# Kernel optimization log

Hardware: AMD Instinct MI355X
Metric: run time of the kernel (lower is better)

Reference implementation:

```python
import jax, jax.numpy as jnp
import numpy as np

T, B, D = 2048, 16, 1024
DELTA_INIT = -2.0

def _xavier(key, shape, gain=1.0):
    fan_in, fan_out = shape[1], shape[0]
    limit = gain * np.sqrt(6.0 / (fan_in + fan_out))
    return jax.random.uniform(key, shape, jnp.float32, -limit, limit)

def setup_inputs() -> dict:
    key = jax.random.key(0)
    ks = jax.random.split(key, 4)
    return {
        "x": jax.random.normal(ks[0], (T, B, D), jnp.float32),
        "h0": jnp.zeros((B, D), jnp.float32),
        "W_x": _xavier(ks[1], (D, D)),
        "r_h": jnp.zeros((D,), jnp.float32),
        "W_delta": _xavier(ks[2], (D, D), gain=0.1),
        "W_gate": _xavier(ks[3], (D, D)),
        "b": jnp.zeros((D,), jnp.float32),
        "b_delta": jnp.full((D,), DELTA_INIT, jnp.float32),
        "b_gate": jnp.zeros((D,), jnp.float32),
    }

def reference(x, h0, W_x, r_h, W_delta, W_gate, b, b_delta, b_gate):
    # Precompute input projections as batched GEMMs (independent of h):
    delta = jax.nn.sigmoid(jnp.einsum('tbd,ed->tbe', x, W_delta) + b_delta)  # [T,B,D]
    cand_x = jnp.einsum('tbd,ed->tbe', x, W_x) + b                            # [T,B,D]
    gate = jax.nn.silu(jnp.einsum('tbd,ed->tbe', x, W_gate) + b_gate)        # [T,B,D]

    def step(h_prev, inp):
        d_t, cx_t = inp
        cand = jnp.tanh(cx_t + r_h * h_prev)
        h_new = (1.0 - d_t) * h_prev + d_t * cand
        return h_new, h_new

    _, h_seq = jax.lax.scan(step, h0, (delta, cand_x))  # h_seq: [T,B,D]
    output = h_seq * gate
    h = jnp.concatenate([h0[None], h_seq], axis=0)  # [T+1,B,D]
    return output, h
```

## Files before the change

### kernel.cpp

```cpp
#include <hip/hip_runtime.h>
#include <hip/hip_bf16.h>

#define T_DIM 2048
#define B_DIM 16
#define D_DIM 1024
#define M_DIM (T_DIM * B_DIM)
#define K_DIM D_DIM
#define N_DIM (3 * D_DIM)
#define BD (B_DIM * D_DIM)
#define CHUNKS 64
#define CLEN (T_DIM / CHUNKS)
#define NT (K_DIM / 64)

typedef __attribute__((ext_vector_type(8))) short bf16x8;
typedef __attribute__((ext_vector_type(4))) float f32x4;
typedef __attribute__((ext_vector_type(4))) unsigned short us4;
typedef __attribute__((ext_vector_type(8))) unsigned short us8;

__device__ __forceinline__ unsigned short f2bf(float f) {
    unsigned int u = __builtin_bit_cast(unsigned int, f);
    u += 0x7fffu + ((u >> 16) & 1u);
    return (unsigned short)(u >> 16);
}
__device__ __forceinline__ float bf2f(unsigned short s) {
    unsigned int u = ((unsigned int)s) << 16;
    return __builtin_bit_cast(float, u);
}
__device__ __forceinline__ float sigmoid_f(float x) {
    return __builtin_amdgcn_rcpf(1.0f + __expf(-x));
}
__device__ __forceinline__ float tanh_f(float x) {
    float e = __expf(2.0f * x);
    return 1.0f - 2.0f * __builtin_amdgcn_rcpf(e + 1.0f);
}

__device__ __forceinline__ void gload_lds16(const unsigned short* g, unsigned short* l) {
    __builtin_amdgcn_global_load_lds(
        (const __attribute__((address_space(1))) unsigned int*)g,
        (__attribute__((address_space(3))) unsigned int*)l, 16, 0, 0);
}

__device__ __forceinline__ bf16x8 lds_rd(const unsigned short* lds, int slot, int srow, int kk, int lk) {
    int ce = (((kk * 64) + (lk * 16)) ^ ((srow & 7) << 4)) >> 1;
    return *reinterpret_cast<const bf16x8*>(lds + slot * 8192 + srow * 64 + ce);
}

#define XN8 (M_DIM * K_DIM / 8)
#define WN8 (D_DIM * K_DIM / 8)
__global__ __launch_bounds__(256)
void conv_all(const float* __restrict__ x,  const float* __restrict__ Wx,
              const float* __restrict__ Wd, const float* __restrict__ Wg,
              unsigned short* __restrict__ xb, unsigned short* __restrict__ Wb)
{
    int i = blockIdx.x * 256 + threadIdx.x;
    const float* src;
    unsigned short* dst;
    int off;
    if (i < XN8)                { src = x;  dst = xb;               off = i; }
    else if (i < XN8 + WN8)     { src = Wx; dst = Wb;               off = i - XN8; }
    else if (i < XN8 + 2 * WN8) { src = Wd; dst = Wb + (size_t)WN8 * 8;     off = i - XN8 - WN8; }
    else                        { src = Wg; dst = Wb + (size_t)2 * WN8 * 8; off = i - XN8 - 2 * WN8; }
    const f32x4* p = reinterpret_cast<const f32x4*>(src) + (size_t)off * 2;
    f32x4 v0 = __builtin_nontemporal_load(p);
    f32x4 v1 = __builtin_nontemporal_load(p + 1);
    us8 w;
    w[0] = f2bf(v0[0]); w[1] = f2bf(v0[1]); w[2] = f2bf(v0[2]); w[3] = f2bf(v0[3]);
    w[4] = f2bf(v1[0]); w[5] = f2bf(v1[1]); w[6] = f2bf(v1[2]); w[7] = f2bf(v1[3]);
    *reinterpret_cast<us8*>(dst + (size_t)off * 8) = w;
}

__global__ __launch_bounds__(512, 2)
void gemm_fused(const unsigned short* __restrict__ xb,
                const unsigned short* __restrict__ Wb,
                const float* __restrict__ bx, const float* __restrict__ bdl,
                const float* __restrict__ bg,
                unsigned short* __restrict__ cxw, unsigned short* __restrict__ dw,
                unsigned short* __restrict__ gw)
{
    __shared__ unsigned short lds[8 * 8192];
    unsigned short* ldsA = lds;
    unsigned short* ldsB = lds + 4 * 8192;

    const int NWG = (M_DIM / 256) * (N_DIM / 256);
    int bid = blockIdx.x;
    int wg  = (bid & 7) * (NWG / 8) + (bid >> 3);
    const int bidM = wg / 12;
    const int bidN = wg % 12;
    const int tM  = bidM * 256;
    const int tN  = bidN * 256;
    const int arr = tN >> 10;
    const int nb  = tN & 1023;

    const float* bias = (arr == 0) ? bx : (arr == 1) ? bdl : bg;
    unsigned short* outp = (arr == 0) ? cxw : (arr == 1) ? dw : gw;

    const int tid  = threadIdx.x;
    const int lane = tid & 63;
    const int wid  = tid >> 6;
    const int wr = wid >> 2, wc = wid & 3;
    const int lr = lane & 15, lk = lane >> 4;

    const unsigned short* Asrc = xb + (size_t)tM * K_DIM;
    const unsigned short* Bsrc = Wb + (size_t)arr * (D_DIM * K_DIM) + (size_t)nb * K_DIM;

    const int t8 = tid >> 3;
    const int ke = (((tid & 7) ^ (t8 & 7)) << 3);
    auto arow = [&](int h, int w) {
        int s = w * 64 + t8;
        return ((s >> 4) & 1) * 128 + (h * 4 + (s >> 5)) * 16 + (s & 15);
    };
    const int rA00 = arow(0, 0), rA01 = arow(0, 1);
    const int rA10 = arow(1, 0), rA11 = arow(1, 1);

    auto stA = [&](int t, int r0, int r1, int slot) {
        gload_lds16(Asrc + (size_t)r0 * K_DIM + t * 64 + ke, ldsA + slot * 8192 + wid * 512);
        gload_lds16(Asrc + (size_t)r1 * K_DIM + t * 64 + ke, ldsA + slot * 8192 + 4096 + wid * 512);
    };
    auto stB = [&](int t, int h, int slot) {
        gload_lds16(Bsrc + (size_t)(h * 128 + t8) * K_DIM + t * 64 + ke,      ldsB + slot * 8192 + wid * 512);
        gload_lds16(Bsrc + (size_t)(h * 128 + 64 + t8) * K_DIM + t * 64 + ke, ldsB + slot * 8192 + 4096 + wid * 512);
    };

    f32x4 acc[8][4];
#pragma unroll
    for (int mi = 0; mi < 8; mi++)
#pragma unroll
        for (int ni = 0; ni < 4; ni++)
            acc[mi][ni] = (f32x4){0.f, 0.f, 0.f, 0.f};

    stA(0, rA00, rA01, 0);
    stA(0, rA10, rA11, 1);
    stB(0, 0, 0);
    stB(0, 1, 1);
    stB(1, 0, 2);
    stA(1, rA00, rA01, 2);
    stB(1, 1, 3);
    asm volatile("s_waitcnt vmcnt(6)" ::: "memory");
    __builtin_amdgcn_s_barrier();

    const int brow = (wc & 1) * 64;
    bf16x8 bf[4][2], afP[2][2], afQ[2][2];

#define RD_AF(DST, P, ASLOT)                                                       \
    do {                                                                           \
        _Pragma("unroll") for (int j = 0; j < 2; j++)                              \
            _Pragma("unroll") for (int kk = 0; kk < 2; kk++)                       \
                DST[j][kk] = lds_rd(ldsA, (ASLOT),                                 \
                                    ((2 * (P) + j) & 3) * 32 + wr * 16 + lr, kk, lk); \
    } while (0)

#define RD_BF(BSLOT)                                                               \
    do {                                                                           \
        _Pragma("unroll") for (int ni = 0; ni < 4; ni++)                           \
            _Pragma("unroll") for (int kk = 0; kk < 2; kk++)                       \
                bf[ni][kk] = lds_rd(ldsB, (BSLOT), brow + ni * 16 + lr, kk, lk);   \
    } while (0)

#define MFMA8(P, AF)                                                               \
    do {                                                                           \
        __builtin_amdgcn_s_setprio(1);                                             \
        _Pragma("unroll") for (int j = 0; j < 2; j++)                              \
            _Pragma("unroll") for (int ni = 0; ni < 4; ni++) {                     \
                acc[2 * (P) + j][ni] = __builtin_amdgcn_mfma_f32_16x16x32_bf16(    \
                    bf[ni][0], AF[j][0], acc[2 * (P) + j][ni], 0, 0, 0);           \
                acc[2 * (P) + j][ni] = __builtin_amdgcn_mfma_f32_16x16x32_bf16(    \
                    bf[ni][1], AF[j][1], acc[2 * (P) + j][ni], 0, 0, 0);           \
            }                                                                      \
        __builtin_amdgcn_s_setprio(0);                                             \
    } while (0)

#define SCHED0 __builtin_amdgcn_sched_barrier(0)
#define BAR    __builtin_amdgcn_s_barrier()

#define TILE(KT, PAR, LAST)                                                        \
    do {                                                                           \
        const int a0s = 2 * (PAR), a1s = 2 * (PAR) + 1;                            \
             \
        if ((KT) + 1 < NT) stA((KT) + 1, rA10, rA11, 2 * (1 - (PAR)) + 1);         \
        RD_AF(afQ, 1, a0s);                                                        \
        SCHED0;                                                                    \
        MFMA8(0, afP);                                                             \
        BAR;                                                                       \
                                                                          \
        if ((KT) + 2 < NT) stB((KT) + 2, 0, 2 * (PAR));                            \
        RD_AF(afP, 2, a1s);                                                        \
        SCHED0;                                                                    \
        MFMA8(1, afQ);                                                             \
        BAR;                                                                       \
                                                                          \
        if ((KT) + 2 < NT) stA((KT) + 2, rA00, rA01, 2 * (PAR));                   \
        RD_AF(afQ, 3, a1s);                                                        \
        SCHED0;                                                                    \
        MFMA8(2, afP);                                                             \
        BAR;                                                                       \
           \
           \
        if ((KT) + 2 < NT) stB((KT) + 2, 1, 2 * (PAR) + 1);                        \
        if ((KT) < NT - 2) asm volatile("s_waitcnt vmcnt(6)" ::: "memory");        \
        else               asm volatile("s_waitcnt vmcnt(0)" ::: "memory");        \
        BAR;                                                                       \
        MFMA8(3, afQ);                                                             \
        if (!(LAST)) {                                                             \
            RD_BF(2 * (1 - (PAR)) + (wc >> 1));                                    \
            RD_AF(afP, 0, 2 * (1 - (PAR)));                                        \
        }                                                                          \
        BAR;                                                                       \
    } while (0)

    RD_BF(wc >> 1);
    RD_AF(afP, 0, 0);

    for (int kt = 0; kt < NT; kt += 2) {
        TILE(kt, 0, false);
        TILE(kt + 1, 1, (kt + 1 == NT - 1));
    }

#pragma unroll
    for (int mi = 0; mi < 8; mi++) {
        int row = wr * 128 + mi * 16 + lr;
#pragma unroll
        for (int ni = 0; ni < 4; ni++) {
            int col0 = wc * 64 + ni * 16 + lk * 4;
            f32x4 bia = *reinterpret_cast<const f32x4*>(bias + nb + col0);
            us4 w;
#pragma unroll
            for (int r = 0; r < 4; r++) {
                float v = acc[mi][ni][r] + bia[r];
                if (arr == 1)      v = sigmoid_f(v);
                else if (arr == 2) v = v * sigmoid_f(v);
                w[r] = f2bf(v);
            }
            int byte = (row * 512 + col0 * 2) ^ ((row & 7) << 4);
            *reinterpret_cast<us4*>(reinterpret_cast<char*>(lds) + byte) = w;
        }
    }
    __syncthreads();
#pragma unroll
    for (int it = 0; it < 16; ++it) {
        int off8 = it * 512 + tid;
        int row  = off8 >> 5;
        int col8 = (off8 & 31) << 3;
        int byte = (row * 512 + col8 * 2) ^ ((row & 7) << 4);
        us8 v = *reinterpret_cast<const us8*>(reinterpret_cast<char*>(lds) + byte);
        __builtin_nontemporal_store(v,
            reinterpret_cast<us8*>(outp + (size_t)(tM + row) * D_DIM + nb + col8));
    }
#undef RD_AF
#undef RD_BF
#undef MFMA8
#undef SCHED0
#undef BAR
#undef TILE
}

__global__ __launch_bounds__(256)
void scan_pass1(const unsigned short* __restrict__ dw,
                const unsigned short* __restrict__ cxw,
                float* __restrict__ Aw, float* __restrict__ Bw)
{
    int g  = blockIdx.x * 256 + threadIdx.x;
    int c  = g / (BD / 4);
    int i0 = (g % (BD / 4)) * 4;
    size_t base = (size_t)c * CLEN * BD + i0;

    float a[4]  = {1.f, 1.f, 1.f, 1.f};
    float hb[4] = {0.f, 0.f, 0.f, 0.f};
    for (int t = 0; t < CLEN; t++) {
        us4 dv = *reinterpret_cast<const us4*>(dw  + base + (size_t)t * BD);
        us4 cv = *reinterpret_cast<const us4*>(cxw + base + (size_t)t * BD);
#pragma unroll
        for (int j = 0; j < 4; j++) {
            float d = bf2f(dv[j]);
            float om = 1.f - d;
            float cand = tanh_f(bf2f(cv[j]));
            hb[j] = om * hb[j] + d * cand;
            a[j] *= om;
        }
    }
    f32x4 av = {a[0], a[1], a[2], a[3]};
    f32x4 bv = {hb[0], hb[1], hb[2], hb[3]};
    *reinterpret_cast<f32x4*>(Aw + (size_t)c * BD + i0) = av;
    *reinterpret_cast<f32x4*>(Bw + (size_t)c * BD + i0) = bv;
}

__global__ __launch_bounds__(256)
void scan_pass2(const float* __restrict__ Aw, const float* __restrict__ Bw,
                const float* __restrict__ h0, float* __restrict__ hin,
                float* __restrict__ hseq)
{
    int i0 = (blockIdx.x * 256 + threadIdx.x) * 4;
    if (i0 >= BD) return;
    f32x4 h = *reinterpret_cast<const f32x4*>(h0 + i0);
    *reinterpret_cast<f32x4*>(hseq + i0) = h;
    for (int c = 0; c < CHUNKS; c++) {
        *reinterpret_cast<f32x4*>(hin + (size_t)c * BD + i0) = h;
        f32x4 A  = *reinterpret_cast<const f32x4*>(Aw + (size_t)c * BD + i0);
        f32x4 Bv = *reinterpret_cast<const f32x4*>(Bw + (size_t)c * BD + i0);
        h = A * h + Bv;
    }
}

__global__ __launch_bounds__(256)
void scan_pass3(const unsigned short* __restrict__ dw,
                const unsigned short* __restrict__ cxw,
                const unsigned short* __restrict__ gw,
                const float* __restrict__ hin,
                float* __restrict__ out, float* __restrict__ hseq)
{
    int g  = blockIdx.x * 256 + threadIdx.x;
    int c  = g / (BD / 4);
    int i0 = (g % (BD / 4)) * 4;
    size_t base = (size_t)c * CLEN * BD + i0;

    f32x4 h4 = *reinterpret_cast<const f32x4*>(hin + (size_t)c * BD + i0);
    float h[4] = {h4[0], h4[1], h4[2], h4[3]};
    for (int t = 0; t < CLEN; t++) {
        size_t idx = base + (size_t)t * BD;
        us4 dv = *reinterpret_cast<const us4*>(dw  + idx);
        us4 cv = *reinterpret_cast<const us4*>(cxw + idx);
        us4 gv = *reinterpret_cast<const us4*>(gw  + idx);
        f32x4 o, hv;
#pragma unroll
        for (int j = 0; j < 4; j++) {
            float d = bf2f(dv[j]);
            float om = 1.f - d;
            float cand = tanh_f(bf2f(cv[j]));
            h[j] = om * h[j] + d * cand;
            o[j] = h[j] * bf2f(gv[j]);
            hv[j] = h[j];
        }
        __builtin_nontemporal_store(o,  reinterpret_cast<f32x4*>(out + idx));
        __builtin_nontemporal_store(hv, reinterpret_cast<f32x4*>(hseq + idx + BD));
    }
}

__global__ __launch_bounds__(256)
void scan_fixup(const float* __restrict__ rh, const float* __restrict__ h0,
                const unsigned short* __restrict__ dw,
                const unsigned short* __restrict__ cxw,
                const unsigned short* __restrict__ gw,
                float* __restrict__ out, float* __restrict__ hseq)
{
    int i = blockIdx.x * 256 + threadIdx.x;
    if (i >= BD) return;
    float r = rh[i & (D_DIM - 1)];
    if (r == 0.0f) return;
    float h = h0[i];
    for (int t = 0; t < T_DIM; t++) {
        size_t idx = (size_t)t * BD + i;
        float d = bf2f(dw[idx]);
        float cand = tanh_f(bf2f(cxw[idx]) + r * h);
        h = (1.f - d) * h + d * cand;
        out[idx] = h * bf2f(gw[idx]);
        hseq[idx + BD] = h;
    }
}

extern "C" void kernel_launch(void* const* d_in, const int* in_sizes, int n_in,
                              void* d_out, int out_size, void* d_ws, size_t ws_size,
                              hipStream_t stream)
{
    const float* x   = (const float*)d_in[0];
    const float* h0  = (const float*)d_in[1];
    const float* Wx  = (const float*)d_in[2];
    const float* rh  = (const float*)d_in[3];
    const float* Wd  = (const float*)d_in[4];
    const float* Wg  = (const float*)d_in[5];
    const float* bx  = (const float*)d_in[6];
    const float* bdl = (const float*)d_in[7];
    const float* bg  = (const float*)d_in[8];

    float* out  = (float*)d_out;
    float* hseq = out + (size_t)T_DIM * BD;

    unsigned short* dw  = (unsigned short*)d_ws;
    unsigned short* cxw = dw  + (size_t)M_DIM * D_DIM;
    unsigned short* gw  = cxw + (size_t)M_DIM * D_DIM;
    float* Aw  = (float*)(gw + (size_t)M_DIM * D_DIM);
    float* Bw  = Aw + (size_t)CHUNKS * BD;
    float* hin = Bw + (size_t)CHUNKS * BD;

    unsigned short* xb = (unsigned short*)d_out;
    unsigned short* Wb = xb + (size_t)M_DIM * K_DIM;

    conv_all<<<dim3((XN8 + 3 * WN8) / 256), dim3(256), 0, stream>>>(x, Wx, Wd, Wg, xb, Wb);

    gemm_fused<<<dim3((M_DIM / 256) * (N_DIM / 256)), dim3(512), 0, stream>>>(
        xb, Wb, bx, bdl, bg, cxw, dw, gw);

    scan_pass1<<<dim3(CHUNKS * BD / 4 / 256), dim3(256), 0, stream>>>(dw, cxw, Aw, Bw);
    scan_pass2<<<dim3(BD / 4 / 256 + 1), dim3(256), 0, stream>>>(Aw, Bw, h0, hin, hseq);
    scan_pass3<<<dim3(CHUNKS * BD / 4 / 256), dim3(256), 0, stream>>>(dw, cxw, gw, hin, out, hseq);
    scan_fixup<<<dim3(BD / 256), dim3(256), 0, stream>>>(rh, h0, dw, cxw, gw, out, hseq);
}
```

Baseline: 373.4 us.

## Collapse GEMM k-tile pipeline into two phases with full A-fragment loads

Restructures the bf16 MFMA main loop of the projection GEMM. The old version used four phases per k-tile, ping-ponging A fragments between two register sets and separating phases with sched barriers. The new version has two phases: it loads all four A fragments for one half of the tile, then issues 32 MFMAs, and groups the next-tile A/B global-to-LDS loads into one block. This cuts barriers per tile and drops the scheduling fences, but gives up the explicit overlap of LDS reads with MFMA work and raises register pressure. The prologue now waits for all outstanding loads instead of leaving some in flight.

```diff
diff --git a/kernel.cpp b/kernel.cpp
--- a/kernel.cpp
+++ b/kernel.cpp
@@ -132,21 +132,20 @@
     stA(0, rA10, rA11, 1);
     stB(0, 0, 0);
     stB(0, 1, 1);
+    stA(1, rA00, rA01, 2);
     stB(1, 0, 2);
-    stA(1, rA00, rA01, 2);
     stB(1, 1, 3);
-    asm volatile("s_waitcnt vmcnt(6)" ::: "memory");
+    asm volatile("s_waitcnt vmcnt(0)" ::: "memory");
     __builtin_amdgcn_s_barrier();
 
     const int brow = (wc & 1) * 64;
-    bf16x8 bf[4][2], afP[2][2], afQ[2][2];
-
-#define RD_AF(DST, P, ASLOT)                                                       \
+    bf16x8 bf[4][2], af[4][2];
+
+#define RD_AF8(ASLOT)                                                              \
     do {                                                                           \
-        _Pragma("unroll") for (int j = 0; j < 2; j++)                              \
+        _Pragma("unroll") for (int m4 = 0; m4 < 4; m4++)                           \
             _Pragma("unroll") for (int kk = 0; kk < 2; kk++)                       \
-                DST[j][kk] = lds_rd(ldsA, (ASLOT),                                 \
-                                    ((2 * (P) + j) & 3) * 32 + wr * 16 + lr, kk, lk); \
+                af[m4][kk] = lds_rd(ldsA, (ASLOT), m4 * 32 + wr * 16 + lr, kk, lk); \
     } while (0)
 
 #define RD_BF(BSLOT)                                                               \
@@ -156,59 +155,44 @@
                 bf[ni][kk] = lds_rd(ldsB, (BSLOT), brow + ni * 16 + lr, kk, lk);   \
     } while (0)
 
-#define MFMA8(P, AF)                                                               \
+#define MFMA32(HALF)                                                               \
     do {                                                                           \
         __builtin_amdgcn_s_setprio(1);                                             \
-        _Pragma("unroll") for (int j = 0; j < 2; j++)                              \
+        _Pragma("unroll") for (int m4 = 0; m4 < 4; m4++)                           \
             _Pragma("unroll") for (int ni = 0; ni < 4; ni++) {                     \
-                acc[2 * (P) + j][ni] = __builtin_amdgcn_mfma_f32_16x16x32_bf16(    \
-                    bf[ni][0], AF[j][0], acc[2 * (P) + j][ni], 0, 0, 0);           \
-                acc[2 * (P) + j][ni] = __builtin_amdgcn_mfma_f32_16x16x32_bf16(    \
-                    bf[ni][1], AF[j][1], acc[2 * (P) + j][ni], 0, 0, 0);           \
+                acc[(HALF) * 4 + m4][ni] = __builtin_amdgcn_mfma_f32_16x16x32_bf16( \
+                    bf[ni][0], af[m4][0], acc[(HALF) * 4 + m4][ni], 0, 0, 0);      \
+                acc[(HALF) * 4 + m4][ni] = __builtin_amdgcn_mfma_f32_16x16x32_bf16( \
+                    bf[ni][1], af[m4][1], acc[(HALF) * 4 + m4][ni], 0, 0, 0);      \
             }                                                                      \
         __builtin_amdgcn_s_setprio(0);                                             \
     } while (0)
 
-#define SCHED0 __builtin_amdgcn_sched_barrier(0)
-#define BAR    __builtin_amdgcn_s_barrier()
+#define BAR __builtin_amdgcn_s_barrier()
 
 #define TILE(KT, PAR, LAST)                                                        \
     do {                                                                           \
         const int a0s = 2 * (PAR), a1s = 2 * (PAR) + 1;                            \
+                            \
+        if ((KT) + 1 < NT) stA((KT) + 1, rA10, rA11, 2 * (1 - (PAR)) + 1);         \
+        RD_AF8(a0s);                                                               \
+        MFMA32(0);                                                                 \
+        BAR;                                                                       \
              \
-        if ((KT) + 1 < NT) stA((KT) + 1, rA10, rA11, 2 * (1 - (PAR)) + 1);         \
-        RD_AF(afQ, 1, a0s);                                                        \
-        SCHED0;                                                                    \
-        MFMA8(0, afP);                                                             \
-        BAR;                                                                       \
-                                                                          \
-        if ((KT) + 2 < NT) stB((KT) + 2, 0, 2 * (PAR));                            \
-        RD_AF(afP, 2, a1s);                                                        \
-        SCHED0;                                                                    \
-        MFMA8(1, afQ);                                                             \
-        BAR;                                                                       \
-                                                                          \
-        if ((KT) + 2 < NT) stA((KT) + 2, rA00, rA01, 2 * (PAR));                   \
-        RD_AF(afQ, 3, a1s);                                                        \
-        SCHED0;                                                                    \
-        MFMA8(2, afP);                                                             \
-        BAR;                                                                       \
-           \
-           \
-        if ((KT) + 2 < NT) stB((KT) + 2, 1, 2 * (PAR) + 1);                        \
+        if ((KT) + 2 < NT) {                                                       \
+            stA((KT) + 2, rA00, rA01, a0s);                                        \
+            stB((KT) + 2, 0, a0s);                                                 \
+            stB((KT) + 2, 1, a1s);                                                 \
+        }                                                                          \
+        RD_AF8(a1s);                                                               \
+        MFMA32(1);                                                                 \
         if ((KT) < NT - 2) asm volatile("s_waitcnt vmcnt(6)" ::: "memory");        \
         else               asm volatile("s_waitcnt vmcnt(0)" ::: "memory");        \
         BAR;                                                                       \
-        MFMA8(3, afQ);                                                             \
-        if (!(LAST)) {                                                             \
-            RD_BF(2 * (1 - (PAR)) + (wc >> 1));                                    \
-            RD_AF(afP, 0, 2 * (1 - (PAR)));                                        \
-        }                                                                          \
-        BAR;                                                                       \
+        if (!(LAST)) RD_BF(2 * (1 - (PAR)) + (wc >> 1));                           \
     } while (0)
 
     RD_BF(wc >> 1);
-    RD_AF(afP, 0, 0);
 
     for (int kt = 0; kt < NT; kt += 2) {
         TILE(kt, 0, false);
@@ -245,10 +229,9 @@
         __builtin_nontemporal_store(v,
             reinterpret_cast<us8*>(outp + (size_t)(tM + row) * D_DIM + nb + col8));
     }
-#undef RD_AF
+#undef RD_AF8
 #undef RD_BF
-#undef MFMA8
-#undef SCHED0
+#undef MFMA32
 #undef BAR
 #undef TILE
 }
```

Result: no change. 371.2 us (-0.6%).
